# Kernel tuning notes

Measured on AMD Instinct MI355X. Metric: run time of the kernel, lower is better.

## Reference

```python
import jax, jax.numpy as jnp
import numpy as np

MARGIN = 0.3
N, D = 4096, 512
NUM_CLASSES = 64

def setup_inputs() -> dict:
    key = jax.random.key(0)
    k1, k2, k3 = jax.random.split(key, 3)
    src_feat = jax.random.normal(k1, (N, D), dtype=jnp.float32)
    tgt_feat = jax.random.normal(k2, (N, D), dtype=jnp.float32)
    labels = jax.random.randint(k3, (N,), 0, NUM_CLASSES, dtype=jnp.int64)
    return {"src_feat": src_feat, "tgt_feat": tgt_feat, "labels": labels}

def reference(src_feat, tgt_feat, labels):
    # squared Euclidean distance matrix [n, n]
    e1 = jnp.sum(src_feat * src_feat, axis=1, keepdims=True)   # [n,1]
    e2 = jnp.sum(tgt_feat * tgt_feat, axis=1, keepdims=True).T  # [1,n]
    dist = e1 + e2 - 2.0 * (src_feat @ tgt_feat.T)
    dist = jnp.maximum(dist, 0.0)  # matches dist_mat[dist_mat < 0] = 0
    # same-label mask [n, n]
    mask = labels[:, None] == labels[None, :]
    # hard positive: max dist among same-label cols; hard negative: min among others
    dist_ap = jnp.max(jnp.where(mask, dist, -jnp.inf), axis=1)  # [n]
    dist_an = jnp.min(jnp.where(mask, jnp.inf, dist), axis=1)   # [n]
    # MarginRankingLoss with target y = 1: mean(relu(-(an - ap) + margin))
    loss = jnp.mean(jax.nn.relu(dist_ap - dist_an + MARGIN))
    return loss
```

## Files before the change

### kernel.cpp

```cpp
#include <hip/hip_runtime.h>
#include <hip/hip_bf16.h>
#include <stdint.h>

#define N_PTS 4096
#define DIM 512
#define MARGIN_F 0.3f
#define POS_INF_BITS 0x7f800000

typedef short bf16x8 __attribute__((ext_vector_type(8)));
typedef float f32x4 __attribute__((ext_vector_type(4)));

__device__ __forceinline__ unsigned short f2bf(float f) {
    unsigned int b = __float_as_uint(f);
    b += 0x7FFF + ((b >> 16) & 1);
    return (unsigned short)(b >> 16);
}

__device__ __forceinline__ void async16(const unsigned short* g, unsigned short* l) {
    __builtin_amdgcn_global_load_lds(
        (const __attribute__((address_space(1))) unsigned int*)g,
        (__attribute__((address_space(3))) unsigned int*)l,
        16, 0, 0);
}

#define RAW_BARRIER()  asm volatile("s_barrier" ::: "memory")
#define WAIT_VM8()     asm volatile("s_waitcnt vmcnt(8)" ::: "memory")
#define WAIT_VM4()     asm volatile("s_waitcnt vmcnt(4)" ::: "memory")
#define WAIT_VM0()     asm volatile("s_waitcnt vmcnt(0)" ::: "memory")

__global__ __launch_bounds__(256) void prep_kernel(
    const float* __restrict__ src, const float* __restrict__ tgt,
    unsigned short* __restrict__ src_bf, unsigned short* __restrict__ tgt_bf,
    float* __restrict__ e1, float* __restrict__ e2,
    float* __restrict__ out)
{
    const int row  = blockIdx.x * 4 + (threadIdx.x >> 6);
    const int lane = threadIdx.x & 63;

    if (blockIdx.x == 0 && threadIdx.x == 0) out[0] = 0.0f;

    const float4* s4 = (const float4*)(src + (size_t)row * DIM);
    const float4* t4 = (const float4*)(tgt + (size_t)row * DIM);
    float4 a0 = s4[lane], a1 = s4[lane + 64];
    float4 b0 = t4[lane], b1 = t4[lane + 64];

    ushort4 u;
    ushort4* so = (ushort4*)(src_bf + (size_t)row * DIM);
    ushort4* to = (ushort4*)(tgt_bf + (size_t)row * DIM);
    u.x = f2bf(a0.x); u.y = f2bf(a0.y); u.z = f2bf(a0.z); u.w = f2bf(a0.w); so[lane] = u;
    u.x = f2bf(a1.x); u.y = f2bf(a1.y); u.z = f2bf(a1.z); u.w = f2bf(a1.w); so[lane + 64] = u;
    u.x = f2bf(b0.x); u.y = f2bf(b0.y); u.z = f2bf(b0.z); u.w = f2bf(b0.w); to[lane] = u;
    u.x = f2bf(b1.x); u.y = f2bf(b1.y); u.z = f2bf(b1.z); u.w = f2bf(b1.w); to[lane + 64] = u;

    float s1 = a0.x*a0.x + a0.y*a0.y + a0.z*a0.z + a0.w*a0.w
             + a1.x*a1.x + a1.y*a1.y + a1.z*a1.z + a1.w*a1.w;
    float s2 = b0.x*b0.x + b0.y*b0.y + b0.z*b0.z + b0.w*b0.w
             + b1.x*b1.x + b1.y*b1.y + b1.z*b1.z + b1.w*b1.w;
    for (int off = 32; off; off >>= 1) {
        s1 += __shfl_down(s1, off);
        s2 += __shfl_down(s2, off);
    }
    if (lane == 0) {
        e1[row] = s1;
        e2[row] = s2;
    }
}

#define BM 128
#define BN 128
#define BK 32
#define NSTEP (DIM / BK)
#define NPART 64

__global__ __launch_bounds__(256) void dist_kernel(
    const unsigned short* __restrict__ src_bf,
    const unsigned short* __restrict__ tgt_bf,
    const float* __restrict__ e1, const float* __restrict__ e2,
    const int* __restrict__ labels,
    float* __restrict__ ap_part, float* __restrict__ an_part)
{
    __shared__ unsigned short As[3][BM * BK];
    __shared__ unsigned short Bs[3][BN * BK];
    __shared__ int   li[BM];
    __shared__ int   lj[BN];
    __shared__ float e1s[BM];
    __shared__ float e2s[BN];

    const int i0 = blockIdx.y * BM;
    const int j0 = blockIdx.x * BN;
    const int t = threadIdx.x;
    const int lane = t & 63;
    const int wave = t >> 6;

    if (t < BM) { li[t] = labels[i0 + t]; e1s[t] = e1[i0 + t]; }
    else        { int u = t - BM; lj[u] = labels[j0 + u]; e2s[u] = e2[j0 + u]; }

    const int srow = t >> 2;
    const int scol = ((t & 3) ^ ((srow >> 1) & 3)) * 8;
    const unsigned short* gA0 = src_bf + (size_t)(i0 + srow) * DIM + scol;
    const unsigned short* gA1 = src_bf + (size_t)(i0 + 64 + srow) * DIM + scol;
    const unsigned short* gB0 = tgt_bf + (size_t)(j0 + srow) * DIM + scol;
    const unsigned short* gB1 = tgt_bf + (size_t)(j0 + 64 + srow) * DIM + scol;
    const int ldsOff0 = wave * 512;
    const int ldsOff1 = 2048 + wave * 512;

    const int wm = (wave >> 1) * 64;
    const int wn = (wave & 1) * 64;
    const int fr = lane & 15;
    const int quad = lane >> 4;
    const int fkey = (fr >> 1) & 3;
    const int cp = (quad ^ fkey) * 8;

    f32x4 acc[4][4];
    #pragma unroll
    for (int a = 0; a < 4; a++)
        #pragma unroll
        for (int b = 0; b < 4; b++)
            acc[a][b] = (f32x4){0.f, 0.f, 0.f, 0.f};

    #pragma unroll
    for (int p = 0; p < 2; p++) {
        const int kk = p * BK;
        async16(gA0 + kk, &As[p][0] + ldsOff0);
        async16(gA1 + kk, &As[p][0] + ldsOff1);
        async16(gB0 + kk, &Bs[p][0] + ldsOff0);
        async16(gB1 + kk, &Bs[p][0] + ldsOff1);
    }

    #pragma unroll
    for (int s = 0; s < NSTEP; s++) {
        if (s + 2 < NSTEP) {
            const int kk = (s + 2) * BK;
            const int nb = (s + 2) % 3;
            async16(gA0 + kk, &As[nb][0] + ldsOff0);
            async16(gA1 + kk, &As[nb][0] + ldsOff1);
            async16(gB0 + kk, &Bs[nb][0] + ldsOff0);
            async16(gB1 + kk, &Bs[nb][0] + ldsOff1);
            WAIT_VM8();
        } else if (s + 2 == NSTEP) {
            WAIT_VM4();
        } else {
            WAIT_VM0();
        }
        RAW_BARRIER();

        const unsigned short* aa = &As[s % 3][0];
        const unsigned short* bb = &Bs[s % 3][0];
        bf16x8 af[4], bf[4];
        #pragma unroll
        for (int x = 0; x < 4; x++) {
            af[x] = *(const bf16x8*)&aa[(wm + x * 16 + fr) * BK + cp];
            bf[x] = *(const bf16x8*)&bb[(wn + x * 16 + fr) * BK + cp];
        }
        #pragma unroll
        for (int tm = 0; tm < 4; tm++)
            #pragma unroll
            for (int tn = 0; tn < 4; tn++)
                acc[tm][tn] = __builtin_amdgcn_mfma_f32_16x16x32_bf16(
                    af[tm], bf[tn], acc[tm][tn], 0, 0, 0);

        if (s + 1 < NSTEP)
            RAW_BARRIER();
    }

    const float INF = __int_as_float(POS_INF_BITS);
    const int pcol = blockIdx.x * 2 + (wave & 1);
    #pragma unroll
    for (int tm = 0; tm < 4; tm++) {
        #pragma unroll
        for (int r = 0; r < 4; r++) {
            const int rl = wm + tm * 16 + quad * 4 + r;
            const float e1v = e1s[rl];
            const int   liv = li[rl];
            float apv = 0.0f;
            float anv = INF;
            #pragma unroll
            for (int tn = 0; tn < 4; tn++) {
                const int cl = wn + tn * 16 + fr;
                float d = e1v + e2s[cl] - 2.0f * acc[tm][tn][r];
                d = fmaxf(d, 0.0f);
                if (liv == lj[cl]) apv = fmaxf(apv, d);
                else               anv = fminf(anv, d);
            }
            #pragma unroll
            for (int off = 1; off < 16; off <<= 1) {
                apv = fmaxf(apv, __shfl_xor(apv, off));
                anv = fminf(anv, __shfl_xor(anv, off));
            }
            if (fr == 0) {
                ap_part[(size_t)(i0 + rl) * NPART + pcol] = apv;
                an_part[(size_t)(i0 + rl) * NPART + pcol] = anv;
            }
        }
    }
}

__global__ __launch_bounds__(128) void loss_kernel(
    const float* __restrict__ ap_part, const float* __restrict__ an_part,
    float* __restrict__ out)
{
    const int row = blockIdx.x * 128 + threadIdx.x;
    const float4* a4 = (const float4*)(ap_part + (size_t)row * NPART);
    const float4* n4 = (const float4*)(an_part + (size_t)row * NPART);
    float apv = 0.0f;
    float anv = __int_as_float(POS_INF_BITS);
    #pragma unroll
    for (int i = 0; i < NPART / 4; i++) {
        float4 a = a4[i], n = n4[i];
        apv = fmaxf(apv, fmaxf(fmaxf(a.x, a.y), fmaxf(a.z, a.w)));
        anv = fminf(anv, fminf(fminf(n.x, n.y), fminf(n.z, n.w)));
    }
    float s = fmaxf(apv - anv + MARGIN_F, 0.0f);
    for (int off = 32; off; off >>= 1) s += __shfl_down(s, off);
    __shared__ float red[2];
    if ((threadIdx.x & 63) == 0) red[threadIdx.x >> 6] = s;
    __syncthreads();
    if (threadIdx.x == 0)
        atomicAdd(out, (red[0] + red[1]) / (float)N_PTS);
}

extern "C" void kernel_launch(void* const* d_in, const int* in_sizes, int n_in,
                              void* d_out, int out_size, void* d_ws, size_t ws_size,
                              hipStream_t stream) {
    const float* src   = (const float*)d_in[0];
    const float* tgt   = (const float*)d_in[1];
    const int* labels  = (const int*)d_in[2];

    char* ws = (char*)d_ws;
    const size_t featB = (size_t)N_PTS * DIM * sizeof(unsigned short);
    unsigned short* src_bf = (unsigned short*)ws;
    unsigned short* tgt_bf = (unsigned short*)(ws + featB);
    float* e1 = (float*)(ws + 2 * featB);
    float* e2 = e1 + N_PTS;
    float* ap_part = e2 + N_PTS;
    float* an_part = ap_part + (size_t)N_PTS * NPART;

    prep_kernel<<<N_PTS / 4, 256, 0, stream>>>(src, tgt, src_bf, tgt_bf,
                                               e1, e2, (float*)d_out);
    dim3 grid(N_PTS / BN, N_PTS / BM);
    dist_kernel<<<grid, 256, 0, stream>>>(src_bf, tgt_bf, e1, e2, labels,
                                          ap_part, an_part);
    loss_kernel<<<N_PTS / 128, 128, 0, stream>>>(ap_part, an_part, (float*)d_out);
}
```

Measured before the change: 102.6 us.

## Widen distance tile to 128x256 with each wave owning a 128x64 strip

Doubles the column tile of the distance GEMM to 256, so each of the four waves computes all 128 rows against its own 64 columns. Each loaded A tile is now reused across twice as many columns, and the per-block load count and wait thresholds are adjusted to match. The cost is a doubled accumulator footprint (32 MFMA tiles per wave), more LDS per block, and half as many blocks for a 4096x4096 problem, which may limit occupancy. The launch bound now also requests two blocks per multiprocessor.

```diff
diff --git a/kernel.cpp b/kernel.cpp
--- a/kernel.cpp
+++ b/kernel.cpp
@@ -24,8 +24,8 @@
 }
 
 #define RAW_BARRIER()  asm volatile("s_barrier" ::: "memory")
-#define WAIT_VM8()     asm volatile("s_waitcnt vmcnt(8)" ::: "memory")
-#define WAIT_VM4()     asm volatile("s_waitcnt vmcnt(4)" ::: "memory")
+#define WAIT_VM12()    asm volatile("s_waitcnt vmcnt(12)" ::: "memory")
+#define WAIT_VM6()     asm volatile("s_waitcnt vmcnt(6)" ::: "memory")
 #define WAIT_VM0()     asm volatile("s_waitcnt vmcnt(0)" ::: "memory")
 
 __global__ __launch_bounds__(256) void prep_kernel(
@@ -67,12 +67,12 @@
 }
 
 #define BM 128
-#define BN 128
+#define BN 256
 #define BK 32
 #define NSTEP (DIM / BK)
 #define NPART 64
 
-__global__ __launch_bounds__(256) void dist_kernel(
+__global__ __launch_bounds__(256, 2) void dist_kernel(
     const unsigned short* __restrict__ src_bf,
     const unsigned short* __restrict__ tgt_bf,
     const float* __restrict__ e1, const float* __restrict__ e2,
@@ -92,8 +92,9 @@
     const int lane = t & 63;
     const int wave = t >> 6;
 
+    lj[t] = labels[j0 + t];
+    e2s[t] = e2[j0 + t];
     if (t < BM) { li[t] = labels[i0 + t]; e1s[t] = e1[i0 + t]; }
-    else        { int u = t - BM; lj[u] = labels[j0 + u]; e2s[u] = e2[j0 + u]; }
 
     const int srow = t >> 2;
     const int scol = ((t & 3) ^ ((srow >> 1) & 3)) * 8;
@@ -101,19 +102,24 @@
     const unsigned short* gA1 = src_bf + (size_t)(i0 + 64 + srow) * DIM + scol;
     const unsigned short* gB0 = tgt_bf + (size_t)(j0 + srow) * DIM + scol;
     const unsigned short* gB1 = tgt_bf + (size_t)(j0 + 64 + srow) * DIM + scol;
-    const int ldsOff0 = wave * 512;
-    const int ldsOff1 = 2048 + wave * 512;
-
-    const int wm = (wave >> 1) * 64;
-    const int wn = (wave & 1) * 64;
+    const unsigned short* gB2 = tgt_bf + (size_t)(j0 + 128 + srow) * DIM + scol;
+    const unsigned short* gB3 = tgt_bf + (size_t)(j0 + 192 + srow) * DIM + scol;
+    const int aOff0 = wave * 512;
+    const int aOff1 = 2048 + wave * 512;
+    const int bOff0 = wave * 512;
+    const int bOff1 = 2048 + wave * 512;
+    const int bOff2 = 4096 + wave * 512;
+    const int bOff3 = 6144 + wave * 512;
+
+    const int wn = wave * 64;
     const int fr = lane & 15;
     const int quad = lane >> 4;
     const int fkey = (fr >> 1) & 3;
     const int cp = (quad ^ fkey) * 8;
 
-    f32x4 acc[4][4];
-    #pragma unroll
-    for (int a = 0; a < 4; a++)
+    f32x4 acc[8][4];
+    #pragma unroll
+    for (int a = 0; a < 8; a++)
         #pragma unroll
         for (int b = 0; b < 4; b++)
             acc[a][b] = (f32x4){0.f, 0.f, 0.f, 0.f};
@@ -121,10 +127,12 @@
     #pragma unroll
     for (int p = 0; p < 2; p++) {
         const int kk = p * BK;
-        async16(gA0 + kk, &As[p][0] + ldsOff0);
-        async16(gA1 + kk, &As[p][0] + ldsOff1);
-        async16(gB0 + kk, &Bs[p][0] + ldsOff0);
-        async16(gB1 + kk, &Bs[p][0] + ldsOff1);
+        async16(gA0 + kk, &As[p][0] + aOff0);
+        async16(gA1 + kk, &As[p][0] + aOff1);
+        async16(gB0 + kk, &Bs[p][0] + bOff0);
+        async16(gB1 + kk, &Bs[p][0] + bOff1);
+        async16(gB2 + kk, &Bs[p][0] + bOff2);
+        async16(gB3 + kk, &Bs[p][0] + bOff3);
     }
 
     #pragma unroll
@@ -132,13 +140,15 @@
         if (s + 2 < NSTEP) {
             const int kk = (s + 2) * BK;
             const int nb = (s + 2) % 3;
-            async16(gA0 + kk, &As[nb][0] + ldsOff0);
-            async16(gA1 + kk, &As[nb][0] + ldsOff1);
-            async16(gB0 + kk, &Bs[nb][0] + ldsOff0);
-            async16(gB1 + kk, &Bs[nb][0] + ldsOff1);
-            WAIT_VM8();
+            async16(gA0 + kk, &As[nb][0] + aOff0);
+            async16(gA1 + kk, &As[nb][0] + aOff1);
+            async16(gB0 + kk, &Bs[nb][0] + bOff0);
+            async16(gB1 + kk, &Bs[nb][0] + bOff1);
+            async16(gB2 + kk, &Bs[nb][0] + bOff2);
+            async16(gB3 + kk, &Bs[nb][0] + bOff3);
+            WAIT_VM12();
         } else if (s + 2 == NSTEP) {
-            WAIT_VM4();
+            WAIT_VM6();
         } else {
             WAIT_VM0();
         }
@@ -146,14 +156,15 @@
 
         const unsigned short* aa = &As[s % 3][0];
         const unsigned short* bb = &Bs[s % 3][0];
-        bf16x8 af[4], bf[4];
-        #pragma unroll
-        for (int x = 0; x < 4; x++) {
-            af[x] = *(const bf16x8*)&aa[(wm + x * 16 + fr) * BK + cp];
+        bf16x8 af[8], bf[4];
+        #pragma unroll
+        for (int x = 0; x < 8; x++)
+            af[x] = *(const bf16x8*)&aa[(x * 16 + fr) * BK + cp];
+        #pragma unroll
+        for (int x = 0; x < 4; x++)
             bf[x] = *(const bf16x8*)&bb[(wn + x * 16 + fr) * BK + cp];
-        }
-        #pragma unroll
-        for (int tm = 0; tm < 4; tm++)
+        #pragma unroll
+        for (int tm = 0; tm < 8; tm++)
             #pragma unroll
             for (int tn = 0; tn < 4; tn++)
                 acc[tm][tn] = __builtin_amdgcn_mfma_f32_16x16x32_bf16(
@@ -164,12 +175,12 @@
     }
 
     const float INF = __int_as_float(POS_INF_BITS);
-    const int pcol = blockIdx.x * 2 + (wave & 1);
-    #pragma unroll
-    for (int tm = 0; tm < 4; tm++) {
+    const int pcol = blockIdx.x * 4 + wave;
+    #pragma unroll
+    for (int tm = 0; tm < 8; tm++) {
         #pragma unroll
         for (int r = 0; r < 4; r++) {
-            const int rl = wm + tm * 16 + quad * 4 + r;
+            const int rl = tm * 16 + quad * 4 + r;
             const float e1v = e1s[rl];
             const int   liv = li[rl];
             float apv = 0.0f;
```

After: 100.8 us (median of 2 runs). No clear change (-1.8%).
